# Kernel optimization log

Hardware: AMD Instinct MI355X
Metric: run time of the kernel (lower is better)

The kernel has to match this reference:

```python
import jax, jax.numpy as jnp
import numpy as np

EPS = 1e-06
LAMBDA_PCSL = 0.1
LAMBDA_GPAL = 0.1


def setup_inputs() -> dict:
    key = jax.random.key(0)
    k1, k2 = jax.random.split(key)
    N, D, P = 262144, 256, 512
    features = jax.random.normal(k1, (N, D), dtype=jnp.float32)
    patient_ids = jax.random.randint(k2, (N,), 0, P, dtype=jnp.int64)
    return {"features": features, "patient_ids": patient_ids, "num_patients": P}


def _pafa_loss(features, patient_ids, num_patients):
    # Segmented mean: centroids[p] = mean of features with patient_ids == p
    seg_ids = patient_ids.astype(jnp.int32)
    sums = jax.ops.segment_sum(features, seg_ids, num_segments=num_patients)  # [P, D]
    counts = jax.ops.segment_sum(jnp.ones((features.shape[0],), features.dtype),
                                 seg_ids, num_segments=num_patients)          # [P]
    counts = jnp.maximum(counts, 1.0)  # every patient assumed present (as in original)
    centroids = sums / counts[:, None]                                        # [P, D]

    # Within-patient variance: sum_i ||x_i - c_{pid_i}||^2
    diff = features - centroids[seg_ids]                                      # [N, D]
    within_variance = jnp.sum(diff * diff)

    # Pairwise centroid distances: sum_{i<j} ||c_i - c_j||^2
    #   = P * sum_i ||c_i||^2 - ||sum_i c_i||^2   (exact identity, no O(P^2) loop)
    sq_norms = jnp.sum(centroids * centroids, axis=1)                         # [P]
    total = jnp.sum(centroids, axis=0)                                        # [D]
    P = jnp.asarray(num_patients, centroids.dtype)
    between_distance = P * jnp.sum(sq_norms) - jnp.sum(total * total)

    loss_pcsl = within_variance / (between_distance + EPS)

    # Global patient alignment: mean ||c_p - mean(c)||^2
    global_centroid = jnp.mean(centroids, axis=0)                             # [D]
    gdiff = centroids - global_centroid
    loss_gpal = jnp.mean(jnp.sum(gdiff * gdiff, axis=1))

    return LAMBDA_PCSL * loss_pcsl + LAMBDA_GPAL * loss_gpal


def reference(features, patient_ids, num_patients):
    return _pafa_loss(features, patient_ids, num_patients)
```

## Files before the change

### kernel.cpp

```cpp
#include <hip/hip_runtime.h>


#define DIMS 256
#define NPAT 512
#define HB 64
#define HT 1024
#define MT 1024
#define MW 16

extern "C" __global__ void __launch_bounds__(HT)
k_hist(const int* __restrict__ pids, int N, unsigned* __restrict__ bh)
{
    __shared__ unsigned h[NPAT];
    const int t = threadIdx.x;
    if (t < NPAT) h[t] = 0u;
    __syncthreads();

    const int r = (blockIdx.x * HT + t) * 4;
    if (r + 3 < N) {
        const int4 p4 = *reinterpret_cast<const int4*>(pids + r);
        atomicAdd(&h[p4.x], 1u);
        atomicAdd(&h[p4.y], 1u);
        atomicAdd(&h[p4.z], 1u);
        atomicAdd(&h[p4.w], 1u);
    } else {
        for (int k = 0; k < 4; ++k)
            if (r + k < N) atomicAdd(&h[pids[r + k]], 1u);
    }
    __syncthreads();
    if (t < NPAT) bh[t * HB + blockIdx.x] = h[t];
}

extern "C" __global__ void __launch_bounds__(NPAT)
k_scan(unsigned* __restrict__ bh, unsigned* __restrict__ counts,
       unsigned* __restrict__ starts, float* __restrict__ scalars,
       float* __restrict__ T)
{
    __shared__ unsigned tmp[NPAT];
    const int t = threadIdx.x;

    uint4* row = reinterpret_cast<uint4*>(bh + t * HB);
    unsigned run = 0u;
    #pragma unroll
    for (int k = 0; k < HB / 4; ++k) {
        const uint4 v = row[k];
        uint4 e;
        e.x = run;
        e.y = e.x + v.x;
        e.z = e.y + v.y;
        e.w = e.z + v.z;
        run = e.w + v.w;
        row[k] = e;
    }
    counts[t] = run;
    const unsigned padded = (run + 3u) & ~3u;
    tmp[t] = padded;
    __syncthreads();
    for (int off = 1; off < NPAT; off <<= 1) {
        const unsigned v = (t >= off) ? tmp[t - off] : 0u;
        __syncthreads();
        tmp[t] += v;
        __syncthreads();
    }
    starts[t] = tmp[t] - padded;

    if (t < 4)    scalars[t] = 0.0f;
    if (t < DIMS) T[t]       = 0.0f;
}

extern "C" __global__ void __launch_bounds__(HT)
k_scatter(const int* __restrict__ pids, int N,
          const unsigned* __restrict__ bh, const unsigned* __restrict__ starts,
          unsigned* __restrict__ idx)
{
    __shared__ unsigned basec[NPAT];
    const int t = threadIdx.x;
    if (t < NPAT) basec[t] = starts[t] + bh[t * HB + blockIdx.x];
    __syncthreads();

    const int r = (blockIdx.x * HT + t) * 4;
    if (r + 3 < N) {
        const int4 p4 = *reinterpret_cast<const int4*>(pids + r);
        idx[atomicAdd(&basec[p4.x], 1u)] = (unsigned)(r + 0);
        idx[atomicAdd(&basec[p4.y], 1u)] = (unsigned)(r + 1);
        idx[atomicAdd(&basec[p4.z], 1u)] = (unsigned)(r + 2);
        idx[atomicAdd(&basec[p4.w], 1u)] = (unsigned)(r + 3);
    } else {
        for (int k = 0; k < 4; ++k)
            if (r + k < N)
                idx[atomicAdd(&basec[pids[r + k]], 1u)] = (unsigned)(r + k);
    }
}

extern "C" __global__ void __launch_bounds__(MT, 4)
k_main(const float* __restrict__ feats, const unsigned* __restrict__ idx,
       const unsigned* __restrict__ counts, const unsigned* __restrict__ starts,
       float* __restrict__ T, float* __restrict__ scalars)
{
    __shared__ float part[MW][DIMS];
    __shared__ float sred[MW];
    __shared__ float cred[4];

    const int p    = blockIdx.x;
    const int lane = threadIdx.x & 63;
    const int w    = threadIdx.x >> 6;
    const unsigned start = starts[p];
    const unsigned cnt   = counts[p];
    const unsigned base  = lane * 4;

    float ax = 0.f, ay = 0.f, az = 0.f, aw = 0.f;
    float ssq = 0.f;

    const unsigned nb = cnt >> 2;
    for (unsigned b = (unsigned)w; b < nb; b += MW) {
        const uint4 cid = *reinterpret_cast<const uint4*>(idx + start + 4u * b);
        const float4 v0 = *reinterpret_cast<const float4*>(feats + (size_t)cid.x * DIMS + base);
        const float4 v1 = *reinterpret_cast<const float4*>(feats + (size_t)cid.y * DIMS + base);
        const float4 v2 = *reinterpret_cast<const float4*>(feats + (size_t)cid.z * DIMS + base);
        const float4 v3 = *reinterpret_cast<const float4*>(feats + (size_t)cid.w * DIMS + base);
        ax += v0.x + v1.x + v2.x + v3.x;
        ay += v0.y + v1.y + v2.y + v3.y;
        az += v0.z + v1.z + v2.z + v3.z;
        aw += v0.w + v1.w + v2.w + v3.w;
        ssq += v0.x*v0.x + v0.y*v0.y + v0.z*v0.z + v0.w*v0.w;
        ssq += v1.x*v1.x + v1.y*v1.y + v1.z*v1.z + v1.w*v1.w;
        ssq += v2.x*v2.x + v2.y*v2.y + v2.z*v2.z + v2.w*v2.w;
        ssq += v3.x*v3.x + v3.y*v3.y + v3.z*v3.z + v3.w*v3.w;
    }
    if (w == 0) {
        for (unsigned r = nb * 4u; r < cnt; ++r) {
            const unsigned row = idx[start + r];
            const float4 v = *reinterpret_cast<const float4*>(feats + (size_t)row * DIMS + base);
            ax += v.x; ay += v.y; az += v.z; aw += v.w;
            ssq += v.x*v.x + v.y*v.y + v.z*v.z + v.w*v.w;
        }
    }

    part[w][base + 0] = ax;
    part[w][base + 1] = ay;
    part[w][base + 2] = az;
    part[w][base + 3] = aw;
    for (int off = 32; off; off >>= 1) ssq += __shfl_down(ssq, off, 64);
    if (lane == 0) sred[w] = ssq;
    __syncthreads();

    const int d = threadIdx.x;
    if (d < DIMS) {
        float s = 0.f;
        #pragma unroll
        for (int ww = 0; ww < MW; ++ww) s += part[ww][d];
        const float cntf = fmaxf((float)cnt, 1.0f);
        const float c = s / cntf;
        atomicAdd(&T[d], c);
        float csq = c * c;
        for (int off = 32; off; off >>= 1) csq += __shfl_down(csq, off, 64);
        if ((d & 63) == 0) cred[d >> 6] = csq;
    }
    __syncthreads();

    if (threadIdx.x == 0) {
        const float s2p = cred[0] + cred[1] + cred[2] + cred[3];
        const float cntf = fmaxf((float)cnt, 1.0f);
        atomicAdd(&scalars[2], s2p);
        atomicAdd(&scalars[1], cntf * s2p);
        float sq = 0.f;
        #pragma unroll
        for (int ww = 0; ww < MW; ++ww) sq += sred[ww];
        atomicAdd(&scalars[0], sq);
    }
}

extern "C" __global__ void __launch_bounds__(DIMS)
k_final(const float* __restrict__ T, const float* __restrict__ scalars,
        const int* __restrict__ nump, float* __restrict__ out)
{
    __shared__ float red[4];
    const int d = threadIdx.x;
    const float t = T[d];
    float tt = t * t;
    for (int off = 32; off; off >>= 1) tt += __shfl_down(tt, off, 64);
    if ((d & 63) == 0) red[d >> 6] = tt;
    __syncthreads();
    if (d == 0) {
        const double TT    = (double)red[0] + red[1] + red[2] + red[3];
        const double SumSq = (double)scalars[0];
        const double S1    = (double)scalars[1];
        const double S2    = (double)scalars[2];
        const double Pd    = (double)(*nump);
        const double within  = SumSq - S1;
        const double between = Pd * S2 - TT;
        const double pcsl = within / (between + 1e-6);
        const double gpal = S2 / Pd - TT / (Pd * Pd);
        out[0] = (float)(0.1 * pcsl + 0.1 * gpal);
    }
}

extern "C" void kernel_launch(void* const* d_in, const int* in_sizes, int n_in,
                              void* d_out, int out_size, void* d_ws, size_t ws_size,
                              hipStream_t stream)
{
    const float* feats = (const float*)d_in[0];
    const int*   pids  = (const int*)d_in[1];
    const int*   nump  = (const int*)d_in[2];
    float*       out   = (float*)d_out;

    const int N = in_sizes[0] / DIMS;

    char* ws = (char*)d_ws;
    unsigned* counts  = (unsigned*)(ws);
    unsigned* starts  = (unsigned*)(ws + 2048);
    float*    scalars = (float*)(ws + 4096);
    float*    T       = (float*)(ws + 4608);
    unsigned* bh      = (unsigned*)(ws + 8192);
    unsigned* idx     = (unsigned*)(ws + 139264);

    k_hist   <<<dim3(HB),   dim3(HT),   0, stream>>>(pids, N, bh);
    k_scan   <<<dim3(1),    dim3(NPAT), 0, stream>>>(bh, counts, starts,
                                                     scalars, T);
    k_scatter<<<dim3(HB),   dim3(HT),   0, stream>>>(pids, N, bh, starts, idx);
    k_main   <<<dim3(NPAT), dim3(MT),   0, stream>>>(feats, idx, counts, starts,
                                                     T, scalars);
    k_final  <<<dim3(1),    dim3(DIMS), 0, stream>>>(T, scalars, nump, out);
}
```

Before: 76.29 us.

## Fuse histogram, scan and scatter into one kernel with last-block grid sync

Merges the three sorting kernels (histogram, single-block scan, scatter) into one kernel. The last block to finish its histogram performs the scan, and the other blocks spin-wait on a global flag before scattering indices, reusing the patient ids they already loaded. This removes two kernel launches and the second pass over patient ids. In exchange it adds a memset launch and depends on all 64 blocks being co-resident for the spin-wait.

```diff
diff --git a/kernel.cpp b/kernel.cpp
--- a/kernel.cpp
+++ b/kernel.cpp
@@ -8,88 +8,109 @@
 #define MT 1024
 #define MW 16
 
+
 extern "C" __global__ void __launch_bounds__(HT)
-k_hist(const int* __restrict__ pids, int N, unsigned* __restrict__ bh)
+k_sort(const int* __restrict__ pids, int N, unsigned* __restrict__ bh,
+       unsigned* __restrict__ counts, unsigned* __restrict__ starts,
+       unsigned* __restrict__ idx, float* __restrict__ scalars,
+       float* __restrict__ T, unsigned* __restrict__ sync)
 {
     __shared__ unsigned h[NPAT];
-    const int t = threadIdx.x;
+    __shared__ unsigned tmp[NPAT];
+    __shared__ unsigned amLastSh;
+
+    const int t   = threadIdx.x;
+    const int blk = blockIdx.x;
+
     if (t < NPAT) h[t] = 0u;
     __syncthreads();
 
-    const int r = (blockIdx.x * HT + t) * 4;
+    const int r = (blk * HT + t) * 4;
+    int4 p4 = make_int4(-1, -1, -1, -1);
     if (r + 3 < N) {
-        const int4 p4 = *reinterpret_cast<const int4*>(pids + r);
+        p4 = *reinterpret_cast<const int4*>(pids + r);
         atomicAdd(&h[p4.x], 1u);
         atomicAdd(&h[p4.y], 1u);
         atomicAdd(&h[p4.z], 1u);
         atomicAdd(&h[p4.w], 1u);
     } else {
-        for (int k = 0; k < 4; ++k)
-            if (r + k < N) atomicAdd(&h[pids[r + k]], 1u);
-    }
-    __syncthreads();
-    if (t < NPAT) bh[t * HB + blockIdx.x] = h[t];
-}
-
-extern "C" __global__ void __launch_bounds__(NPAT)
-k_scan(unsigned* __restrict__ bh, unsigned* __restrict__ counts,
-       unsigned* __restrict__ starts, float* __restrict__ scalars,
-       float* __restrict__ T)
-{
-    __shared__ unsigned tmp[NPAT];
-    const int t = threadIdx.x;
-
-    uint4* row = reinterpret_cast<uint4*>(bh + t * HB);
-    unsigned run = 0u;
-    #pragma unroll
-    for (int k = 0; k < HB / 4; ++k) {
-        const uint4 v = row[k];
-        uint4 e;
-        e.x = run;
-        e.y = e.x + v.x;
-        e.z = e.y + v.y;
-        e.w = e.z + v.z;
-        run = e.w + v.w;
-        row[k] = e;
-    }
-    counts[t] = run;
-    const unsigned padded = (run + 3u) & ~3u;
-    tmp[t] = padded;
-    __syncthreads();
-    for (int off = 1; off < NPAT; off <<= 1) {
-        const unsigned v = (t >= off) ? tmp[t - off] : 0u;
+        if (r + 0 < N) { p4.x = pids[r + 0]; atomicAdd(&h[p4.x], 1u); }
+        if (r + 1 < N) { p4.y = pids[r + 1]; atomicAdd(&h[p4.y], 1u); }
+        if (r + 2 < N) { p4.z = pids[r + 2]; atomicAdd(&h[p4.z], 1u); }
+        if (r + 3 < N) { p4.w = pids[r + 3]; atomicAdd(&h[p4.w], 1u); }
+    }
+    __syncthreads();
+
+    if (t < NPAT)
+        __hip_atomic_store(&bh[t * HB + blk], h[t],
+                           __ATOMIC_RELEASE, __HIP_MEMORY_SCOPE_AGENT);
+    __syncthreads();
+
+    if (t == 0) {
+        const unsigned prev = __hip_atomic_fetch_add(
+            &sync[0], 1u, __ATOMIC_ACQ_REL, __HIP_MEMORY_SCOPE_AGENT);
+        amLastSh = (prev == (unsigned)(HB - 1)) ? 1u : 0u;
+    }
+    __syncthreads();
+
+    if (amLastSh) {
+        unsigned run = 0u;
+        if (t < NPAT) {
+            unsigned* rowp = bh + t * HB;
+            #pragma unroll
+            for (int k = 0; k < HB; k += 4) {
+                const unsigned v0 = __hip_atomic_load(rowp + k + 0, __ATOMIC_RELAXED, __HIP_MEMORY_SCOPE_AGENT);
+                const unsigned v1 = __hip_atomic_load(rowp + k + 1, __ATOMIC_RELAXED, __HIP_MEMORY_SCOPE_AGENT);
+                const unsigned v2 = __hip_atomic_load(rowp + k + 2, __ATOMIC_RELAXED, __HIP_MEMORY_SCOPE_AGENT);
+                const unsigned v3 = __hip_atomic_load(rowp + k + 3, __ATOMIC_RELAXED, __HIP_MEMORY_SCOPE_AGENT);
+                __hip_atomic_store(rowp + k + 0, run, __ATOMIC_RELAXED, __HIP_MEMORY_SCOPE_AGENT); run += v0;
+                __hip_atomic_store(rowp + k + 1, run, __ATOMIC_RELAXED, __HIP_MEMORY_SCOPE_AGENT); run += v1;
+                __hip_atomic_store(rowp + k + 2, run, __ATOMIC_RELAXED, __HIP_MEMORY_SCOPE_AGENT); run += v2;
+                __hip_atomic_store(rowp + k + 3, run, __ATOMIC_RELAXED, __HIP_MEMORY_SCOPE_AGENT); run += v3;
+            }
+            counts[t] = run;
+            tmp[t] = (run + 3u) & ~3u;
+        }
         __syncthreads();
-        tmp[t] += v;
+        for (int off = 1; off < NPAT; off <<= 1) {
+            const unsigned v = (t >= off && t < NPAT) ? tmp[t - off] : 0u;
+            __syncthreads();
+            if (t < NPAT) tmp[t] += v;
+            __syncthreads();
+        }
+        if (t < NPAT) {
+            const unsigned pad = (run + 3u) & ~3u;
+            __hip_atomic_store(&starts[t], tmp[t] - pad,
+                               __ATOMIC_RELEASE, __HIP_MEMORY_SCOPE_AGENT);
+        }
+        if (t < 4)    scalars[t] = 0.0f;
+        if (t < DIMS) T[t]       = 0.0f;
         __syncthreads();
-    }
-    starts[t] = tmp[t] - padded;
-
-    if (t < 4)    scalars[t] = 0.0f;
-    if (t < DIMS) T[t]       = 0.0f;
-}
-
-extern "C" __global__ void __launch_bounds__(HT)
-k_scatter(const int* __restrict__ pids, int N,
-          const unsigned* __restrict__ bh, const unsigned* __restrict__ starts,
-          unsigned* __restrict__ idx)
-{
-    __shared__ unsigned basec[NPAT];
-    const int t = threadIdx.x;
-    if (t < NPAT) basec[t] = starts[t] + bh[t * HB + blockIdx.x];
-    __syncthreads();
-
-    const int r = (blockIdx.x * HT + t) * 4;
-    if (r + 3 < N) {
-        const int4 p4 = *reinterpret_cast<const int4*>(pids + r);
-        idx[atomicAdd(&basec[p4.x], 1u)] = (unsigned)(r + 0);
-        idx[atomicAdd(&basec[p4.y], 1u)] = (unsigned)(r + 1);
-        idx[atomicAdd(&basec[p4.z], 1u)] = (unsigned)(r + 2);
-        idx[atomicAdd(&basec[p4.w], 1u)] = (unsigned)(r + 3);
+        if (t == 0)
+            __hip_atomic_store(&sync[1], 1u,
+                               __ATOMIC_RELEASE, __HIP_MEMORY_SCOPE_AGENT);
     } else {
-        for (int k = 0; k < 4; ++k)
-            if (r + k < N)
-                idx[atomicAdd(&basec[pids[r + k]], 1u)] = (unsigned)(r + k);
-    }
+        if (t == 0) {
+            while (__hip_atomic_load(&sync[1], __ATOMIC_ACQUIRE,
+                                     __HIP_MEMORY_SCOPE_AGENT) == 0u)
+                __builtin_amdgcn_s_sleep(8);
+        }
+        __syncthreads();
+    }
+
+    if (t < NPAT) {
+        const unsigned st = __hip_atomic_load(&starts[t], __ATOMIC_RELAXED,
+                                              __HIP_MEMORY_SCOPE_AGENT);
+        const unsigned of = __hip_atomic_load(&bh[t * HB + blk], __ATOMIC_RELAXED,
+                                              __HIP_MEMORY_SCOPE_AGENT);
+        h[t] = st + of;
+    }
+    __syncthreads();
+
+    if (p4.x >= 0) idx[atomicAdd(&h[p4.x], 1u)] = (unsigned)(r + 0);
+    if (p4.y >= 0) idx[atomicAdd(&h[p4.y], 1u)] = (unsigned)(r + 1);
+    if (p4.z >= 0) idx[atomicAdd(&h[p4.z], 1u)] = (unsigned)(r + 2);
+    if (p4.w >= 0) idx[atomicAdd(&h[p4.w], 1u)] = (unsigned)(r + 3);
 }
 
 extern "C" __global__ void __launch_bounds__(MT, 4)
@@ -128,8 +149,8 @@
         ssq += v3.x*v3.x + v3.y*v3.y + v3.z*v3.z + v3.w*v3.w;
     }
     if (w == 0) {
-        for (unsigned r = nb * 4u; r < cnt; ++r) {
-            const unsigned row = idx[start + r];
+        for (unsigned rr = nb * 4u; rr < cnt; ++rr) {
+            const unsigned row = idx[start + rr];
             const float4 v = *reinterpret_cast<const float4*>(feats + (size_t)row * DIMS + base);
             ax += v.x; ay += v.y; az += v.z; aw += v.w;
             ssq += v.x*v.x + v.y*v.y + v.z*v.z + v.w*v.w;
@@ -211,14 +232,15 @@
     unsigned* starts  = (unsigned*)(ws + 2048);
     float*    scalars = (float*)(ws + 4096);
     float*    T       = (float*)(ws + 4608);
+    unsigned* syncf   = (unsigned*)(ws + 5632);
     unsigned* bh      = (unsigned*)(ws + 8192);
     unsigned* idx     = (unsigned*)(ws + 139264);
 
-    k_hist   <<<dim3(HB),   dim3(HT),   0, stream>>>(pids, N, bh);
-    k_scan   <<<dim3(1),    dim3(NPAT), 0, stream>>>(bh, counts, starts,
-                                                     scalars, T);
-    k_scatter<<<dim3(HB),   dim3(HT),   0, stream>>>(pids, N, bh, starts, idx);
-    k_main   <<<dim3(NPAT), dim3(MT),   0, stream>>>(feats, idx, counts, starts,
-                                                     T, scalars);
-    k_final  <<<dim3(1),    dim3(DIMS), 0, stream>>>(T, scalars, nump, out);
-}
+    hipMemsetAsync(syncf, 0, 2 * sizeof(unsigned), stream);
+
+    k_sort <<<dim3(HB),   dim3(HT),   0, stream>>>(pids, N, bh, counts, starts,
+                                                   idx, scalars, T, syncf);
+    k_main <<<dim3(NPAT), dim3(MT),   0, stream>>>(feats, idx, counts, starts,
+                                                   T, scalars);
+    k_final<<<dim3(1),    dim3(DIMS), 0, stream>>>(T, scalars, nump, out);
+}
```

New measurement: 236.6 us. 3.1x slower.

## Fold scan kernel into scatter by recomputing prefix sums redundantly per block

Applied to the files above, without the earlier changes.

Removes the single-block scan kernel launch. Each scatter block now reads the full per-block histogram, computes its own exclusive prefix and per-patient totals, and runs a block-wide scan to get starts, while block 0 writes counts and starts for later kernels. Zeroing of the accumulators moves into the histogram kernel. This trades one launch and its serialization gap for redundant scan work in all 64 blocks.

```diff
diff --git a/kernel.cpp b/kernel.cpp
--- a/kernel.cpp
+++ b/kernel.cpp
@@ -8,8 +8,10 @@
 #define MT 1024
 #define MW 16
 
+
 extern "C" __global__ void __launch_bounds__(HT)
-k_hist(const int* __restrict__ pids, int N, unsigned* __restrict__ bh)
+k_hist(const int* __restrict__ pids, int N, unsigned* __restrict__ bh,
+       float* __restrict__ scalars, float* __restrict__ T)
 {
     __shared__ unsigned h[NPAT];
     const int t = threadIdx.x;
@@ -29,56 +31,55 @@
     }
     __syncthreads();
     if (t < NPAT) bh[t * HB + blockIdx.x] = h[t];
-}
-
-extern "C" __global__ void __launch_bounds__(NPAT)
-k_scan(unsigned* __restrict__ bh, unsigned* __restrict__ counts,
-       unsigned* __restrict__ starts, float* __restrict__ scalars,
-       float* __restrict__ T)
-{
-    __shared__ unsigned tmp[NPAT];
-    const int t = threadIdx.x;
-
-    uint4* row = reinterpret_cast<uint4*>(bh + t * HB);
-    unsigned run = 0u;
-    #pragma unroll
-    for (int k = 0; k < HB / 4; ++k) {
-        const uint4 v = row[k];
-        uint4 e;
-        e.x = run;
-        e.y = e.x + v.x;
-        e.z = e.y + v.y;
-        e.w = e.z + v.z;
-        run = e.w + v.w;
-        row[k] = e;
-    }
-    counts[t] = run;
-    const unsigned padded = (run + 3u) & ~3u;
-    tmp[t] = padded;
-    __syncthreads();
-    for (int off = 1; off < NPAT; off <<= 1) {
-        const unsigned v = (t >= off) ? tmp[t - off] : 0u;
-        __syncthreads();
-        tmp[t] += v;
-        __syncthreads();
-    }
-    starts[t] = tmp[t] - padded;
-
-    if (t < 4)    scalars[t] = 0.0f;
-    if (t < DIMS) T[t]       = 0.0f;
+
+    if (blockIdx.x == 0) {
+        if (t < 4)    scalars[t] = 0.0f;
+        if (t < DIMS) T[t]       = 0.0f;
+    }
 }
 
 extern "C" __global__ void __launch_bounds__(HT)
 k_scatter(const int* __restrict__ pids, int N,
-          const unsigned* __restrict__ bh, const unsigned* __restrict__ starts,
-          unsigned* __restrict__ idx)
-{
+          const unsigned* __restrict__ bh, unsigned* __restrict__ counts,
+          unsigned* __restrict__ starts, unsigned* __restrict__ idx)
+{
+    __shared__ unsigned tmp[NPAT];
     __shared__ unsigned basec[NPAT];
-    const int t = threadIdx.x;
-    if (t < NPAT) basec[t] = starts[t] + bh[t * HB + blockIdx.x];
-    __syncthreads();
-
-    const int r = (blockIdx.x * HT + t) * 4;
+
+    const int t   = threadIdx.x;
+    const int blk = blockIdx.x;
+
+    unsigned total = 0u, pref = 0u, padded = 0u;
+    if (t < NPAT) {
+        const uint4* row = reinterpret_cast<const uint4*>(bh + t * HB);
+        #pragma unroll
+        for (int k = 0; k < HB / 4; ++k) {
+            const uint4 v = row[k];
+            const int b0 = 4 * k;
+            pref  += (b0 + 0 < blk ? v.x : 0u);
+            pref  += (b0 + 1 < blk ? v.y : 0u);
+            pref  += (b0 + 2 < blk ? v.z : 0u);
+            pref  += (b0 + 3 < blk ? v.w : 0u);
+            total += v.x + v.y + v.z + v.w;
+        }
+        padded = (total + 3u) & ~3u;
+        tmp[t] = padded;
+    }
+    __syncthreads();
+    for (int off = 1; off < NPAT; off <<= 1) {
+        const unsigned v = (t >= off && t < NPAT) ? tmp[t - off] : 0u;
+        __syncthreads();
+        if (t < NPAT) tmp[t] += v;
+        __syncthreads();
+    }
+    if (t < NPAT) {
+        const unsigned st = tmp[t] - padded;
+        basec[t] = st + pref;
+        if (blk == 0) { starts[t] = st; counts[t] = total; }
+    }
+    __syncthreads();
+
+    const int r = (blk * HT + t) * 4;
     if (r + 3 < N) {
         const int4 p4 = *reinterpret_cast<const int4*>(pids + r);
         idx[atomicAdd(&basec[p4.x], 1u)] = (unsigned)(r + 0);
@@ -128,8 +129,8 @@
         ssq += v3.x*v3.x + v3.y*v3.y + v3.z*v3.z + v3.w*v3.w;
     }
     if (w == 0) {
-        for (unsigned r = nb * 4u; r < cnt; ++r) {
-            const unsigned row = idx[start + r];
+        for (unsigned rr = nb * 4u; rr < cnt; ++rr) {
+            const unsigned row = idx[start + rr];
             const float4 v = *reinterpret_cast<const float4*>(feats + (size_t)row * DIMS + base);
             ax += v.x; ay += v.y; az += v.z; aw += v.w;
             ssq += v.x*v.x + v.y*v.y + v.z*v.z + v.w*v.w;
@@ -214,10 +215,9 @@
     unsigned* bh      = (unsigned*)(ws + 8192);
     unsigned* idx     = (unsigned*)(ws + 139264);
 
-    k_hist   <<<dim3(HB),   dim3(HT),   0, stream>>>(pids, N, bh);
-    k_scan   <<<dim3(1),    dim3(NPAT), 0, stream>>>(bh, counts, starts,
-                                                     scalars, T);
-    k_scatter<<<dim3(HB),   dim3(HT),   0, stream>>>(pids, N, bh, starts, idx);
+    k_hist   <<<dim3(HB),   dim3(HT),   0, stream>>>(pids, N, bh, scalars, T);
+    k_scatter<<<dim3(HB),   dim3(HT),   0, stream>>>(pids, N, bh, counts,
+                                                     starts, idx);
     k_main   <<<dim3(NPAT), dim3(MT),   0, stream>>>(feats, idx, counts, starts,
                                                      T, scalars);
     k_final  <<<dim3(1),    dim3(DIMS), 0, stream>>>(T, scalars, nump, out);
```

Result: faster. 69.67 us (median of 2 runs) (-8.7%).
